# Performance work log

Hardware: AMD Instinct MI355X
Metric: run time of the kernel (lower is better)

## Reference

```python
import jax, jax.numpy as jnp
import numpy as np

NUM_GROUPS = 9
POWER_P = 4.0
B = 8192

def setup_inputs() -> dict:
    key = jax.random.key(0)
    k1, k2, k3 = jax.random.split(key, 3)
    return {
        "logits_tox": jax.random.normal(k1, (B, 1), dtype=jnp.float32),
        "y_tox": jax.random.uniform(k2, (B, 1), dtype=jnp.float32),
        "y_id": jax.random.uniform(k3, (B, NUM_GROUPS), dtype=jnp.float32),
    }

def reference(logits_tox, y_tox, y_id):
    logits = logits_tox[:, 0]                      # [B]
    is_toxic = y_tox[:, 0] >= 0.5                  # [B] bool
    # D[i, j] = softplus(-(logits[i] - logits[j])) = softplus(logits[j] - logits[i])
    # row index i plays the 'pos' role, column index j plays the 'neg' role.
    D = jax.nn.softplus(logits[None, :] - logits[:, None])  # [B, B]

    in_group = (y_id >= 0.5).T                     # [G, B]
    tox = is_toxic[None, :]                        # [1, B]
    dt = logits.dtype
    sub_pos = (in_group & tox).astype(dt)          # [G, B]
    sub_neg = (in_group & ~tox).astype(dt)
    bg_pos = (~in_group & tox).astype(dt)
    bg_neg = (~in_group & ~tox).astype(dt)

    # three pair types: (sub_pos, sub_neg), (bg_pos, sub_neg), (sub_pos, bg_neg)
    pos_masks = jnp.stack([sub_pos, bg_pos, sub_pos])   # [3, G, B]
    neg_masks = jnp.stack([sub_neg, sub_neg, bg_neg])   # [3, G, B]

    num = jnp.einsum('tgi,ij,tgj->tg', pos_masks, D, neg_masks)  # [3, G]
    cnt = pos_masks.sum(-1) * neg_masks.sum(-1)                  # [3, G] n_pos*n_neg
    valid = cnt > 0                                              # pair type contributes only if both sides nonempty
    type_loss = num / jnp.maximum(cnt, 1.0)

    n_valid = valid.astype(dt).sum(0)                            # [G]
    group_loss = (type_loss * valid.astype(dt)).sum(0) / jnp.maximum(n_valid, 1.0)
    gv = (n_valid > 0).astype(dt)                                # [G] group validity
    n_groups = jnp.maximum(gv.sum(), 1.0)

    # power-mean aggregation (power_p = 4 > 1)
    mean_p = (jnp.power(group_loss, POWER_P) * gv).sum() / n_groups
    loss = jnp.power(mean_p, 1.0 / POWER_P)
    return jnp.where(gv.sum() > 0, loss, jnp.array(0.0, dt))
```

## Files before the change

kernel.cpp:

```cpp
#include <hip/hip_runtime.h>
#include <math.h>

#define NG 9
#define NBLK 1024
#define JT 32
#define ITILE 512
#define LOG2E 1.4426950408889634f
#define LN2   0.6931471805599453f

typedef float f32x2 __attribute__((ext_vector_type(2)));

__global__ __launch_bounds__(256) void k_classify(
    const float* __restrict__ logits, const float* __restrict__ ytox,
    const float* __restrict__ yid, int B, int* __restrict__ cnts,
    float2* __restrict__ iLM, float2* __restrict__ jLM) {

    __shared__ int wT[4], wN[4], offT[4], offN[4], bT, bN;
    __shared__ int gT[4][NG], gN[4][NG];

    const int tid = threadIdx.x, lane = tid & 63, wave = tid >> 6;
    const int row = blockIdx.x * 256 + tid;
    const bool v = row < B;

    float l = 0.f; bool tox = false, non = false; int m = 0;
    if (v) {
        l = logits[row] * LOG2E;
        tox = ytox[row] >= 0.5f;
        non = !tox;
#pragma unroll
        for (int g = 0; g < NG; ++g)
            if (yid[row * NG + g] >= 0.5f) m |= 1 << g;
    }
    const unsigned long long bTox = __ballot(tox), bNon = __ballot(non);
    const unsigned long long lt = (1ull << lane) - 1ull;
    const int pT = __popcll(bTox & lt), pN = __popcll(bNon & lt);
    if (lane == 0) { wT[wave] = __popcll(bTox); wN[wave] = __popcll(bNon); }
#pragma unroll
    for (int g = 0; g < NG; ++g) {
        const unsigned long long bt = __ballot(tox && ((m >> g) & 1));
        const unsigned long long bn = __ballot(non && ((m >> g) & 1));
        if (lane == 0) { gT[wave][g] = __popcll(bt); gN[wave][g] = __popcll(bn); }
    }
    __syncthreads();
    if (tid == 0) {
        int a = 0, b = 0;
#pragma unroll
        for (int w = 0; w < 4; ++w) { offT[w] = a; a += wT[w]; offN[w] = b; b += wN[w]; }
        bT = atomicAdd(&cnts[0], a);
        bN = atomicAdd(&cnts[1], b);
    }
    __syncthreads();
    if (tox) iLM[bT + offT[wave] + pT] = make_float2(l, __int_as_float(m));
    if (non) jLM[bN + offN[wave] + pN] = make_float2(l, __int_as_float(m));
    if (tid < NG)
        atomicAdd(&cnts[2 + tid], gT[0][tid] + gT[1][tid] + gT[2][tid] + gT[3][tid]);
    else if (tid >= 64 && tid < 64 + NG) {
        const int g = tid - 64;
        atomicAdd(&cnts[11 + g], gN[0][g] + gN[1][g] + gN[2][g] + gN[3][g]);
    }
}

__global__ __launch_bounds__(256, 4) void k_pairs(
    const int* __restrict__ cnts, const float2* __restrict__ iLM,
    const float2* __restrict__ jLM, float* __restrict__ part) {

    __shared__ float2 jS[JT];
    __shared__ float red[4][27];
    __shared__ float acc[27];

    const int tid = threadIdx.x, lane = tid & 63, wave = tid >> 6;
    const int blk = blockIdx.x;
    const int nI = cnts[0], nJ = cnts[1];
    const int nbI = (nI + ITILE - 1) / ITILE;
    const int nbJ = (nJ + JT - 1) / JT;
    const int nT = nbI * nbJ;

    if (tid < 27) acc[tid] = 0.f;

    f32x2 li = {1e30f, 1e30f};
    int mi0 = 0, mi1 = 0;
    f32x2 Ra = {0.f, 0.f};
    f32x2 Rg[NG];
#pragma unroll
    for (int g = 0; g < NG; ++g) Rg[g] = (f32x2){0.f, 0.f};

    auto flush = [&]() {
#pragma unroll
        for (int g = 0; g < NG; ++g) {
            const bool i0 = (mi0 >> g) & 1, i1 = (mi1 >> g) & 1;
            const float r0 = Rg[g].x, r1 = Rg[g].y;
            float x0 = (i0 ? r0 : 0.f) + (i1 ? r1 : 0.f);
            float x1 = (i0 ? 0.f : r0) + (i1 ? 0.f : r1);
            float x2 = (i0 ? (Ra.x - r0) : 0.f) + (i1 ? (Ra.y - r1) : 0.f);
#pragma unroll
            for (int off = 32; off > 0; off >>= 1) {
                x0 += __shfl_xor(x0, off, 64);
                x1 += __shfl_xor(x1, off, 64);
                x2 += __shfl_xor(x2, off, 64);
            }
            if (lane == 0) {
                red[wave][g] = x0; red[wave][NG + g] = x1; red[wave][2 * NG + g] = x2;
            }
        }
        __syncthreads();
        if (tid < 27)
            acc[tid] += red[0][tid] + red[1][tid] + red[2][tid] + red[3][tid];
    };

    int prev_bi = -1;
    for (int t = blk; t < nT; t += NBLK) {
        const int bi = t % nbI, bj = t / nbI;
        if (bi != prev_bi) {
            if (prev_bi >= 0) flush();
            const int k0 = bi * ITILE + tid, k1 = k0 + 256;
            const float2 a0 = (k0 < nI) ? iLM[k0] : make_float2(1e30f, 0.f);
            const float2 a1 = (k1 < nI) ? iLM[k1] : make_float2(1e30f, 0.f);
            li.x = a0.x; mi0 = __float_as_int(a0.y);
            li.y = a1.x; mi1 = __float_as_int(a1.y);
            Ra = (f32x2){0.f, 0.f};
#pragma unroll
            for (int g = 0; g < NG; ++g) Rg[g] = (f32x2){0.f, 0.f};
            prev_bi = bi;
        }
        const int jbeg = bj * JT;
        const int jcnt = min(JT, nJ - jbeg);
        __syncthreads();
        if (tid < jcnt) jS[tid] = jLM[jbeg + tid];
        __syncthreads();
#pragma unroll 2
        for (int k = 0; k < jcnt; ++k) {
            const float2 jv = jS[k];
            const int mj = __builtin_amdgcn_readfirstlane(__float_as_int(jv.y));
            const f32x2 ljv = {jv.x, jv.x};
            const f32x2 d = ljv - li;
            f32x2 e;
            e.x = __builtin_amdgcn_exp2f(d.x);
            e.y = __builtin_amdgcn_exp2f(d.y);
            const f32x2 one = {1.f, 1.f};
            const f32x2 tpe = e + one;
            f32x2 s;
            s.x = __builtin_amdgcn_logf(tpe.x);
            s.y = __builtin_amdgcn_logf(tpe.y);
            Ra = Ra + s;
#pragma unroll
            for (int g = 0; g < NG; ++g) {
                const float bg = ((mj >> g) & 1) ? 1.f : 0.f;
                const f32x2 bgv = {bg, bg};
                Rg[g] = __builtin_elementwise_fma(bgv, s, Rg[g]);
            }
        }
    }
    if (prev_bi >= 0) flush();
    if (tid < 27) part[tid * NBLK + blk] = acc[tid];
}

__global__ __launch_bounds__(512) void k_final(
    const float* __restrict__ part, const int* __restrict__ cnts,
    float* __restrict__ out) {
    __shared__ float fin[27];
    const int tid = threadIdx.x, lane = tid & 63, wave = tid >> 6;
    for (int r = wave; r < 27; r += 8) {
        float s = 0.f;
#pragma unroll
        for (int q = 0; q < NBLK / 64; ++q) s += part[r * NBLK + (q << 6) + lane];
#pragma unroll
        for (int off = 32; off > 0; off >>= 1) s += __shfl_xor(s, off, 64);
        if (lane == 0) fin[r] = s * LN2;
    }
    __syncthreads();
    if (tid == 0) {
        const long long nT64 = cnts[0], nN64 = cnts[1];
        double accd = 0.0; int ngv = 0;
        for (int g = 0; g < NG; ++g) {
            const long long cT = cnts[2 + g], cN = cnts[11 + g];
            const long long c0 = cT * cN;
            const long long c1 = (nT64 - cT) * cN;
            const long long c2 = cT * (nN64 - cN);
            const double t0 = (double)fin[g]          / (double)(c0 > 0 ? c0 : 1);
            const double t1 = (double)fin[NG + g]     / (double)(c1 > 0 ? c1 : 1);
            const double t2 = (double)fin[2 * NG + g] / (double)(c2 > 0 ? c2 : 1);
            const int nv = (c0 > 0) + (c1 > 0) + (c2 > 0);
            const double gl = ((c0 > 0 ? t0 : 0.0) + (c1 > 0 ? t1 : 0.0) +
                               (c2 > 0 ? t2 : 0.0)) / (double)(nv > 0 ? nv : 1);
            if (nv > 0) { const double g2 = gl * gl; accd += g2 * g2; ++ngv; }
        }
        const double mp = accd / (double)(ngv > 0 ? ngv : 1);
        const double loss = sqrt(sqrt(mp));
        out[0] = (float)(ngv > 0 ? loss : 0.0);
    }
}

extern "C" void kernel_launch(void* const* d_in, const int* in_sizes, int n_in,
                              void* d_out, int out_size, void* d_ws, size_t ws_size,
                              hipStream_t stream) {
    const float* logits = (const float*)d_in[0];
    const float* ytox   = (const float*)d_in[1];
    const float* yid    = (const float*)d_in[2];
    const int B = in_sizes[0];

    char* ws = (char*)d_ws;
    int*    cnts = (int*)ws;
    float2* iLM  = (float2*)(ws + 128);
    float2* jLM  = iLM + B;
    float*  part = (float*)(jLM + B);

    hipMemsetAsync(cnts, 0, 20 * sizeof(int), stream);
    k_classify<<<dim3((B + 255) / 256), dim3(256), 0, stream>>>(
        logits, ytox, yid, B, cnts, iLM, jLM);
    k_pairs<<<dim3(NBLK), dim3(256), 0, stream>>>(cnts, iLM, jLM, part);
    k_final<<<dim3(1), dim3(512), 0, stream>>>(part, cnts, (float*)d_out);
}
```

Baseline: 86.23 us.

## Compact classification in a single block and drop the memset and global atomics

The classify kernel now runs as one 1024-thread block that loops over 1024-row slices, keeping running prefix offsets and group counts in shared memory. It writes the header counts directly, so the memset launch and the global atomics go away. One side effect is that the compaction order becomes deterministic. The cost is that classification now runs serially on a single CU, with two barriers per slice, instead of being spread across many blocks.

New measurement: 100.9 us. 17.0% more time.

```diff
diff --git a/kernel.cpp b/kernel.cpp
--- a/kernel.cpp
+++ b/kernel.cpp
@@ -10,58 +10,73 @@
 
 typedef float f32x2 __attribute__((ext_vector_type(2)));
 
-__global__ __launch_bounds__(256) void k_classify(
+__global__ __launch_bounds__(1024) void k_classify(
     const float* __restrict__ logits, const float* __restrict__ ytox,
-    const float* __restrict__ yid, int B, int* __restrict__ cnts,
+    const float* __restrict__ yid, int B, int* __restrict__ hdr,
     float2* __restrict__ iLM, float2* __restrict__ jLM) {
 
-    __shared__ int wT[4], wN[4], offT[4], offN[4], bT, bN;
-    __shared__ int gT[4][NG], gN[4][NG];
+    __shared__ int wT[16], wN[16], oT[16], oN[16];
+    __shared__ int gTs[16][NG], gNs[16][NG];
+    __shared__ int baseT, baseN;
 
     const int tid = threadIdx.x, lane = tid & 63, wave = tid >> 6;
-    const int row = blockIdx.x * 256 + tid;
-    const bool v = row < B;
-
-    float l = 0.f; bool tox = false, non = false; int m = 0;
-    if (v) {
-        l = logits[row] * LOG2E;
-        tox = ytox[row] >= 0.5f;
-        non = !tox;
-#pragma unroll
-        for (int g = 0; g < NG; ++g)
-            if (yid[row * NG + g] >= 0.5f) m |= 1 << g;
-    }
-    const unsigned long long bTox = __ballot(tox), bNon = __ballot(non);
     const unsigned long long lt = (1ull << lane) - 1ull;
-    const int pT = __popcll(bTox & lt), pN = __popcll(bNon & lt);
-    if (lane == 0) { wT[wave] = __popcll(bTox); wN[wave] = __popcll(bNon); }
-#pragma unroll
-    for (int g = 0; g < NG; ++g) {
-        const unsigned long long bt = __ballot(tox && ((m >> g) & 1));
-        const unsigned long long bn = __ballot(non && ((m >> g) & 1));
-        if (lane == 0) { gT[wave][g] = __popcll(bt); gN[wave][g] = __popcll(bn); }
-    }
+
+    if (tid < 16 * NG) { gTs[tid / NG][tid % NG] = 0; gNs[tid / NG][tid % NG] = 0; }
+    if (tid == 0) { baseT = 0; baseN = 0; }
     __syncthreads();
-    if (tid == 0) {
-        int a = 0, b = 0;
-#pragma unroll
-        for (int w = 0; w < 4; ++w) { offT[w] = a; a += wT[w]; offN[w] = b; b += wN[w]; }
-        bT = atomicAdd(&cnts[0], a);
-        bN = atomicAdd(&cnts[1], b);
+
+    const int nSl = (B + 1023) >> 10;
+    for (int u = 0; u < nSl; ++u) {
+        const int row = (u << 10) + tid;
+        const bool v = row < B;
+        float l = 0.f; bool tox = false, non = false; int m = 0;
+        if (v) {
+            l = logits[row] * LOG2E;
+            tox = ytox[row] >= 0.5f;
+            non = !tox;
+#pragma unroll
+            for (int g = 0; g < NG; ++g)
+                if (yid[row * NG + g] >= 0.5f) m |= 1 << g;
+        }
+        const unsigned long long bT = __ballot(tox), bN = __ballot(non);
+        const int pT = __popcll(bT & lt), pN = __popcll(bN & lt);
+        if (lane == 0) { wT[wave] = __popcll(bT); wN[wave] = __popcll(bN); }
+#pragma unroll
+        for (int g = 0; g < NG; ++g) {
+            const unsigned long long bt = __ballot(tox && ((m >> g) & 1));
+            const unsigned long long bn = __ballot(non && ((m >> g) & 1));
+            if (lane == 0) { gTs[wave][g] += __popcll(bt); gNs[wave][g] += __popcll(bn); }
+        }
+        __syncthreads();
+        if (tid == 0) {
+            int a = baseT, b = baseN;
+#pragma unroll
+            for (int w = 0; w < 16; ++w) { oT[w] = a; a += wT[w]; oN[w] = b; b += wN[w]; }
+            baseT = a; baseN = b;
+        }
+        __syncthreads();
+        if (tox) iLM[oT[wave] + pT] = make_float2(l, __int_as_float(m));
+        if (non) jLM[oN[wave] + pN] = make_float2(l, __int_as_float(m));
     }
     __syncthreads();
-    if (tox) iLM[bT + offT[wave] + pT] = make_float2(l, __int_as_float(m));
-    if (non) jLM[bN + offN[wave] + pN] = make_float2(l, __int_as_float(m));
-    if (tid < NG)
-        atomicAdd(&cnts[2 + tid], gT[0][tid] + gT[1][tid] + gT[2][tid] + gT[3][tid]);
-    else if (tid >= 64 && tid < 64 + NG) {
+    if (tid == 0) { hdr[0] = baseT; hdr[1] = baseN; }
+    if (tid < NG) {
+        int s = 0;
+#pragma unroll
+        for (int w = 0; w < 16; ++w) s += gTs[w][tid];
+        hdr[2 + tid] = s;
+    } else if (tid >= 64 && tid < 64 + NG) {
         const int g = tid - 64;
-        atomicAdd(&cnts[11 + g], gN[0][g] + gN[1][g] + gN[2][g] + gN[3][g]);
+        int s = 0;
+#pragma unroll
+        for (int w = 0; w < 16; ++w) s += gNs[w][g];
+        hdr[11 + g] = s;
     }
 }
 
 __global__ __launch_bounds__(256, 4) void k_pairs(
-    const int* __restrict__ cnts, const float2* __restrict__ iLM,
+    const int* __restrict__ hdr, const float2* __restrict__ iLM,
     const float2* __restrict__ jLM, float* __restrict__ part) {
 
     __shared__ float2 jS[JT];
@@ -70,7 +85,7 @@
 
     const int tid = threadIdx.x, lane = tid & 63, wave = tid >> 6;
     const int blk = blockIdx.x;
-    const int nI = cnts[0], nJ = cnts[1];
+    const int nI = hdr[0], nJ = hdr[1];
     const int nbI = (nI + ITILE - 1) / ITILE;
     const int nbJ = (nJ + JT - 1) / JT;
     const int nT = nbI * nbJ;
@@ -155,7 +170,7 @@
 }
 
 __global__ __launch_bounds__(512) void k_final(
-    const float* __restrict__ part, const int* __restrict__ cnts,
+    const float* __restrict__ part, const int* __restrict__ hdr,
     float* __restrict__ out) {
     __shared__ float fin[27];
     const int tid = threadIdx.x, lane = tid & 63, wave = tid >> 6;
@@ -169,10 +184,10 @@
     }
     __syncthreads();
     if (tid == 0) {
-        const long long nT64 = cnts[0], nN64 = cnts[1];
+        const long long nT64 = hdr[0], nN64 = hdr[1];
         double accd = 0.0; int ngv = 0;
         for (int g = 0; g < NG; ++g) {
-            const long long cT = cnts[2 + g], cN = cnts[11 + g];
+            const long long cT = hdr[2 + g], cN = hdr[11 + g];
             const long long c0 = cT * cN;
             const long long c1 = (nT64 - cT) * cN;
             const long long c2 = cT * (nN64 - cN);
@@ -199,14 +214,13 @@
     const int B = in_sizes[0];
 
     char* ws = (char*)d_ws;
-    int*    cnts = (int*)ws;
+    int*    hdr  = (int*)ws;
     float2* iLM  = (float2*)(ws + 128);
     float2* jLM  = iLM + B;
     float*  part = (float*)(jLM + B);
 
-    hipMemsetAsync(cnts, 0, 20 * sizeof(int), stream);
-    k_classify<<<dim3((B + 255) / 256), dim3(256), 0, stream>>>(
-        logits, ytox, yid, B, cnts, iLM, jLM);
-    k_pairs<<<dim3(NBLK), dim3(256), 0, stream>>>(cnts, iLM, jLM, part);
-    k_final<<<dim3(1), dim3(512), 0, stream>>>(part, cnts, (float*)d_out);
-}
+    k_classify<<<dim3(1), dim3(1024), 0, stream>>>(logits, ytox, yid, B,
+                                                   hdr, iLM, jLM);
+    k_pairs<<<dim3(NBLK), dim3(256), 0, stream>>>(hdr, iLM, jLM, part);
+    k_final<<<dim3(1), dim3(512), 0, stream>>>(part, hdr, (float*)d_out);
+}
```
